# Optimization experiments

Measured on AMD Instinct MI355X. Metric: run time of the kernel, lower is better.

## Reference

```python
import jax, jax.numpy as jnp
import numpy as np

B, S, D, T = 32, 2048, 128, 8  # batch, seq, input_size, num_trans


def setup_inputs() -> dict:
    key = jax.random.key(0)
    k0, k1, k2, k3 = jax.random.split(key, 4)
    return {
        "input_data": jax.random.normal(k0, (B, S, D), dtype=jnp.float32),
        # nn.Linear(D, D) weights per transform, stacked: [T, D, D]
        "Wx": jax.random.normal(k1, (T, D, D), dtype=jnp.float32) / np.sqrt(D).astype(np.float32),
        "bx": jax.random.normal(k2, (T, D), dtype=jnp.float32) * 0.01,
        # torch.rand init in original
        "p_vectors": jax.random.uniform(k3, (T, 1, D), dtype=jnp.float32),
    }


def reference(input_data, Wx, bx, p_vectors):
    # Batched version of the Python loop of per-transform Linears.
    # torch Linear computes x @ W.T + b -> contract last dim of x with last dim of W.
    transformed = jnp.einsum('bsd,ted->tbse', input_data, Wx) + bx[:, None, None, :]  # [T,B,S,D]

    # Cosine-similarity gating against prototype vectors p_vectors [T,1,D].
    x_norm = jnp.linalg.norm(input_data, axis=2, keepdims=True)[None]        # [1,B,S,1]
    p_norm = jnp.linalg.norm(p_vectors, axis=2, keepdims=True)[:, None]      # [T,1,1,1]
    dot = jnp.sum(input_data[None] * p_vectors[:, None], axis=3, keepdims=True)  # [T,B,S,1]
    cos = dot / (x_norm * p_norm)
    sim = jax.nn.softmax(cos, axis=0)  # softmax over the T transforms

    # Weighted combine + residual (is_y=False path).
    return jnp.sum(sim * transformed, axis=0) + input_data  # [B,S,D]
```

## Files before the change

kernel.cpp:

```cpp
#include <hip/hip_runtime.h>

#define Tq 8
#define Mq 65536

typedef short bf16x8 __attribute__((ext_vector_type(8)));
typedef float f32x4 __attribute__((ext_vector_type(4)));

static __device__ __forceinline__ unsigned short f2bf(float f) {
    unsigned int u = __float_as_uint(f);
    unsigned int r = (u + 0x7FFFu + ((u >> 16) & 1u)) >> 16;
    return (unsigned short)r;
}

__global__ void prep_kernel(const float* __restrict__ W, const float* __restrict__ p,
                            unsigned short* __restrict__ ws) {
    int b = blockIdx.x;
    if (b < 512) {
        int i = b * 256 + threadIdx.x;
        int j    = i & 7;
        int lane = (i >> 3) & 63;
        int k    = (i >> 9) & 3;
        int n    = (i >> 11) & 7;
        int t    = i >> 14;
        int e = n * 16 + (lane & 15);
        int d = k * 32 + (lane >> 4) * 8 + j;
        float w = W[(t * 128 + e) * 128 + d];
        if (e == d) w += 1.0f;
        ws[i] = f2bf(w);
    } else {
        #pragma unroll
        for (int u = 0; u < 16; u++) {
            int i = u * 256 + threadIdx.x;
            int j    = i & 7;
            int lane = (i >> 3) & 63;
            int k    = i >> 9;
            int l16  = lane & 15;
            int quad = lane >> 4;
            int d = k * 32 + quad * 8 + j;
            float v = (l16 < Tq) ? p[l16 * 128 + d] : 0.0f;
            ws[131072 + i] = f2bf(v);
        }
    }
}

__global__ __launch_bounds__(256, 3) void main_kernel(const float* __restrict__ x,
                                                      const unsigned short* __restrict__ wsw,
                                                      const float* __restrict__ bx,
                                                      const float* __restrict__ p,
                                                      float* __restrict__ out) {
    __shared__ float bxl[Tq][64];
    __shared__ float pinv[Tq];

    int tid  = threadIdx.x;
    int bid  = blockIdx.x;
    int rb   = bid >> 1;
    int cb   = bid & 1;
    int wid  = tid >> 6;
    int lane = tid & 63;
    int l16  = lane & 15;
    int quad = lane >> 4;
    size_t wrow = (size_t)rb * 128 + wid * 32;

    {
        int c  = tid & 63;
        int t2 = tid >> 6;
        bxl[t2][c]     = bx[t2 * 128 + cb * 64 + c];
        bxl[t2 + 4][c] = bx[(t2 + 4) * 128 + cb * 64 + c];
    }
    if (tid < Tq) {
        const f32x4* pg = reinterpret_cast<const f32x4*>(p) + tid * 32;
        float s = 0.f;
        #pragma unroll
        for (int i = 0; i < 32; i++) {
            f32x4 v = pg[i];
            s += v.x * v.x + v.y * v.y + v.z * v.z + v.w * v.w;
        }
        pinv[tid] = rsqrtf(s);
    }

    bf16x8 a[2][4];
    float xinv[2];
    #pragma unroll
    for (int mt = 0; mt < 2; mt++) {
        const f32x4* xr = reinterpret_cast<const f32x4*>(x + (wrow + mt * 16 + l16) * 128);
        float ssq = 0.f;
        #pragma unroll
        for (int k = 0; k < 4; k++) {
            f32x4 v0 = __builtin_nontemporal_load(xr + k * 8 + quad * 2);
            f32x4 v1 = __builtin_nontemporal_load(xr + k * 8 + quad * 2 + 1);
            ssq += v0.x * v0.x + v0.y * v0.y + v0.z * v0.z + v0.w * v0.w
                 + v1.x * v1.x + v1.y * v1.y + v1.z * v1.z + v1.w * v1.w;
            bf16x8 f;
            f[0] = (short)f2bf(v0.x); f[1] = (short)f2bf(v0.y);
            f[2] = (short)f2bf(v0.z); f[3] = (short)f2bf(v0.w);
            f[4] = (short)f2bf(v1.x); f[5] = (short)f2bf(v1.y);
            f[6] = (short)f2bf(v1.z); f[7] = (short)f2bf(v1.w);
            a[mt][k] = f;
        }
        ssq += __shfl_xor(ssq, 16);
        ssq += __shfl_xor(ssq, 32);
        xinv[mt] = rsqrtf(ssq);
    }

    const bf16x8* pf = reinterpret_cast<const bf16x8*>(wsw) + 16384;
    bf16x8 pfrag[4];
    #pragma unroll
    for (int k = 0; k < 4; k++) pfrag[k] = pf[k * 64 + lane];
    f32x4 d[2] = {};
    #pragma unroll
    for (int k = 0; k < 4; k++) {
        d[0] = __builtin_amdgcn_mfma_f32_16x16x32_bf16(a[0][k], pfrag[k], d[0], 0, 0, 0);
        d[1] = __builtin_amdgcn_mfma_f32_16x16x32_bf16(a[1][k], pfrag[k], d[1], 0, 0, 0);
    }

    __syncthreads();

    float pv = pinv[l16 & 7];
    f32x4 sim[2];
    #pragma unroll
    for (int mt = 0; mt < 2; mt++) {
        f32x4 c;
        #pragma unroll
        for (int rr = 0; rr < 4; rr++) {
            float xir = __shfl(xinv[mt], (lane & 48) | (quad * 4 + rr));
            c[rr] = d[mt][rr] * xir * pv;
        }
        f32x4 mx = c;
        #pragma unroll
        for (int m = 1; m <= 4; m <<= 1)
            #pragma unroll
            for (int rr = 0; rr < 4; rr++) mx[rr] = fmaxf(mx[rr], __shfl_xor(mx[rr], m));
        f32x4 e;
        #pragma unroll
        for (int rr = 0; rr < 4; rr++) e[rr] = __expf(c[rr] - mx[rr]);
        f32x4 sm = e;
        #pragma unroll
        for (int m = 1; m <= 4; m <<= 1)
            #pragma unroll
            for (int rr = 0; rr < 4; rr++) sm[rr] += __shfl_xor(sm[rr], m);
        #pragma unroll
        for (int rr = 0; rr < 4; rr++) sim[mt][rr] = e[rr] / sm[rr];
    }

    const bf16x8* wb = reinterpret_cast<const bf16x8*>(wsw);
    int nt0 = cb * 4;
    bf16x8 buf[2][4];
    #pragma unroll
    for (int k = 0; k < 4; k++)
        buf[0][k] = wb[(size_t)((0 * 8 + nt0) * 4 + k) * 64 + lane];

    f32x4 o[2][4] = {};

    #pragma unroll 1
    for (int t = 0; t < Tq; t++) {
        f32x4 s0, s1;
        int src = (lane & 48) | t;
        #pragma unroll
        for (int rr = 0; rr < 4; rr++) {
            s0[rr] = __shfl(sim[0][rr], src);
            s1[rr] = __shfl(sim[1][rr], src);
        }
        #pragma unroll
        for (int n = 0; n < 4; n++) {
            int cur = n & 1;
            {
                int n2 = (n + 1) & 3;
                int t2 = (n == 3) ? ((t + 1) & 7) : t;
                #pragma unroll
                for (int k = 0; k < 4; k++)
                    buf[cur ^ 1][k] = wb[(size_t)((t2 * 8 + nt0 + n2) * 4 + k) * 64 + lane];
            }
            float bias = bxl[t][n * 16 + l16];
            f32x4 y0 = {bias, bias, bias, bias};
            f32x4 y1 = {bias, bias, bias, bias};
            #pragma unroll
            for (int k = 0; k < 4; k++) {
                y0 = __builtin_amdgcn_mfma_f32_16x16x32_bf16(a[0][k], buf[cur][k], y0, 0, 0, 0);
                y1 = __builtin_amdgcn_mfma_f32_16x16x32_bf16(a[1][k], buf[cur][k], y1, 0, 0, 0);
            }
            #pragma unroll
            for (int rr = 0; rr < 4; rr++) {
                o[0][n][rr] += s0[rr] * y0[rr];
                o[1][n][rr] += s1[rr] * y1[rr];
            }
        }
    }

    #pragma unroll
    for (int mt = 0; mt < 2; mt++)
        #pragma unroll
        for (int rr = 0; rr < 4; rr++) {
            size_t row = wrow + mt * 16 + quad * 4 + rr;
            #pragma unroll
            for (int n = 0; n < 4; n++)
                __builtin_nontemporal_store(o[mt][n][rr], out + row * 128 + cb * 64 + n * 16 + l16);
        }
}

extern "C" void kernel_launch(void* const* d_in, const int* in_sizes, int n_in,
                              void* d_out, int out_size, void* d_ws, size_t ws_size,
                              hipStream_t stream) {
    const float* x   = (const float*)d_in[0];
    const float* Wx  = (const float*)d_in[1];
    const float* bx  = (const float*)d_in[2];
    const float* p   = (const float*)d_in[3];
    float* out = (float*)d_out;

    unsigned short* ws = (unsigned short*)d_ws;

    prep_kernel<<<dim3(513), dim3(256), 0, stream>>>(Wx, p, ws);
    main_kernel<<<dim3(Mq / 128 * 2), dim3(256), 0, stream>>>(x, ws, bx, p, out);
}
```

Before: 124.7 us.

## Retile main kernel to 128-row blocks with LDS-staged x and double-buffered weights

Each block now covers 128 full rows instead of splitting output columns across two blocks, so x is read from global memory once instead of twice. x is converted to bf16 and staged in LDS, with row norms accumulated through shared atomics. Each wave computes a 64x64 tile with four M-subtiles. Per-transform weight tiles are brought in with global_load_lds into a double buffer in LDS instead of per-lane global loads. The cost is more registers, lower occupancy (launch bound 3 to 2), half as many blocks, and extra barriers per transform.

```diff
diff --git a/kernel.cpp b/kernel.cpp
--- a/kernel.cpp
+++ b/kernel.cpp
@@ -43,30 +43,28 @@
     }
 }
 
-__global__ __launch_bounds__(256, 3) void main_kernel(const float* __restrict__ x,
+__global__ __launch_bounds__(256, 2) void main_kernel(const float* __restrict__ x,
                                                       const unsigned short* __restrict__ wsw,
                                                       const float* __restrict__ bx,
                                                       const float* __restrict__ p,
                                                       float* __restrict__ out) {
-    __shared__ float bxl[Tq][64];
+    __shared__ unsigned short un[32768];
+    __shared__ float bxl[Tq][128];
+    __shared__ float ssql[128];
     __shared__ float pinv[Tq];
 
     int tid  = threadIdx.x;
-    int bid  = blockIdx.x;
-    int rb   = bid >> 1;
-    int cb   = bid & 1;
     int wid  = tid >> 6;
     int lane = tid & 63;
     int l16  = lane & 15;
     int quad = lane >> 4;
-    size_t wrow = (size_t)rb * 128 + wid * 32;
-
-    {
-        int c  = tid & 63;
-        int t2 = tid >> 6;
-        bxl[t2][c]     = bx[t2 * 128 + cb * 64 + c];
-        bxl[t2 + 4][c] = bx[(t2 + 4) * 128 + cb * 64 + c];
-    }
+    size_t m0 = (size_t)blockIdx.x * 128;
+    int mrow = (wid >> 1) * 64;
+    int nt0  = (wid & 1) * 4;
+    int ncol = (wid & 1) * 64;
+
+    if (tid < 128) ssql[tid] = 0.f;
+    reinterpret_cast<f32x4*>(&bxl[0][0])[tid] = reinterpret_cast<const f32x4*>(bx)[tid];
     if (tid < Tq) {
         const f32x4* pg = reinterpret_cast<const f32x4*>(p) + tid * 32;
         float s = 0.f;
@@ -77,123 +75,148 @@
         }
         pinv[tid] = rsqrtf(s);
     }
-
-    bf16x8 a[2][4];
-    float xinv[2];
-    #pragma unroll
-    for (int mt = 0; mt < 2; mt++) {
-        const f32x4* xr = reinterpret_cast<const f32x4*>(x + (wrow + mt * 16 + l16) * 128);
-        float ssq = 0.f;
-        #pragma unroll
-        for (int k = 0; k < 4; k++) {
-            f32x4 v0 = __builtin_nontemporal_load(xr + k * 8 + quad * 2);
-            f32x4 v1 = __builtin_nontemporal_load(xr + k * 8 + quad * 2 + 1);
-            ssq += v0.x * v0.x + v0.y * v0.y + v0.z * v0.z + v0.w * v0.w
-                 + v1.x * v1.x + v1.y * v1.y + v1.z * v1.z + v1.w * v1.w;
-            bf16x8 f;
-            f[0] = (short)f2bf(v0.x); f[1] = (short)f2bf(v0.y);
-            f[2] = (short)f2bf(v0.z); f[3] = (short)f2bf(v0.w);
-            f[4] = (short)f2bf(v1.x); f[5] = (short)f2bf(v1.y);
-            f[6] = (short)f2bf(v1.z); f[7] = (short)f2bf(v1.w);
-            a[mt][k] = f;
-        }
-        ssq += __shfl_xor(ssq, 16);
-        ssq += __shfl_xor(ssq, 32);
-        xinv[mt] = rsqrtf(ssq);
-    }
+    __syncthreads();
+
+    const f32x4* xg4 = reinterpret_cast<const f32x4*>(x + m0 * 128);
+    #pragma unroll
+    for (int it = 0; it < 16; it++) {
+        int flat = it * 256 + tid;
+        int row = flat >> 5;
+        int c4  = flat & 31;
+        f32x4 v = __builtin_nontemporal_load(xg4 + flat);
+        atomicAdd(&ssql[row], v.x * v.x + v.y * v.y + v.z * v.z + v.w * v.w);
+        ushort4 bv;
+        bv.x = f2bf(v.x); bv.y = f2bf(v.y); bv.z = f2bf(v.z); bv.w = f2bf(v.w);
+        *reinterpret_cast<ushort4*>(&un[row * 136 + c4 * 4]) = bv;
+    }
+    __syncthreads();
+
+    bf16x8 a[4][4];
+    #pragma unroll
+    for (int mt = 0; mt < 4; mt++)
+        #pragma unroll
+        for (int k = 0; k < 4; k++)
+            a[mt][k] = *reinterpret_cast<const bf16x8*>(&un[(mrow + mt * 16 + l16) * 136 + k * 32 + quad * 8]);
+
+    f32x4 xinvv[4];
+    #pragma unroll
+    for (int mt = 0; mt < 4; mt++)
+        #pragma unroll
+        for (int rr = 0; rr < 4; rr++)
+            xinvv[mt][rr] = rsqrtf(ssql[mrow + mt * 16 + quad * 4 + rr]);
 
     const bf16x8* pf = reinterpret_cast<const bf16x8*>(wsw) + 16384;
     bf16x8 pfrag[4];
     #pragma unroll
     for (int k = 0; k < 4; k++) pfrag[k] = pf[k * 64 + lane];
-    f32x4 d[2] = {};
-    #pragma unroll
-    for (int k = 0; k < 4; k++) {
-        d[0] = __builtin_amdgcn_mfma_f32_16x16x32_bf16(a[0][k], pfrag[k], d[0], 0, 0, 0);
-        d[1] = __builtin_amdgcn_mfma_f32_16x16x32_bf16(a[1][k], pfrag[k], d[1], 0, 0, 0);
-    }
+    f32x4 d[4] = {};
+    #pragma unroll
+    for (int k = 0; k < 4; k++)
+        #pragma unroll
+        for (int mt = 0; mt < 4; mt++)
+            d[mt] = __builtin_amdgcn_mfma_f32_16x16x32_bf16(a[mt][k], pfrag[k], d[mt], 0, 0, 0);
 
     __syncthreads();
 
+    const char* wsrc = reinterpret_cast<const char*>(wsw);
+    char* lbase = reinterpret_cast<char*>(un);
+    {
+        #pragma unroll
+        for (int it = 0; it < 8; it++) {
+            int off = it * 4096 + wid * 1024;
+            __builtin_amdgcn_global_load_lds(
+                (const __attribute__((address_space(1))) unsigned int*)(wsrc + off + lane * 16),
+                (__attribute__((address_space(3))) unsigned int*)(lbase + off),
+                16, 0, 0);
+        }
+    }
+
     float pv = pinv[l16 & 7];
-    f32x4 sim[2];
-    #pragma unroll
-    for (int mt = 0; mt < 2; mt++) {
+    f32x4 sim[4];
+    #pragma unroll
+    for (int mt = 0; mt < 4; mt++) {
         f32x4 c;
         #pragma unroll
-        for (int rr = 0; rr < 4; rr++) {
-            float xir = __shfl(xinv[mt], (lane & 48) | (quad * 4 + rr));
-            c[rr] = d[mt][rr] * xir * pv;
-        }
+        for (int rr = 0; rr < 4; rr++) c[rr] = d[mt][rr] * xinvv[mt][rr] * pv;
         f32x4 mx = c;
         #pragma unroll
         for (int m = 1; m <= 4; m <<= 1)
             #pragma unroll
             for (int rr = 0; rr < 4; rr++) mx[rr] = fmaxf(mx[rr], __shfl_xor(mx[rr], m));
-        f32x4 e;
-        #pragma unroll
-        for (int rr = 0; rr < 4; rr++) e[rr] = __expf(c[rr] - mx[rr]);
-        f32x4 sm = e;
+        #pragma unroll
+        for (int rr = 0; rr < 4; rr++) c[rr] = __expf(c[rr] - mx[rr]);
+        f32x4 sm = c;
         #pragma unroll
         for (int m = 1; m <= 4; m <<= 1)
             #pragma unroll
             for (int rr = 0; rr < 4; rr++) sm[rr] += __shfl_xor(sm[rr], m);
         #pragma unroll
-        for (int rr = 0; rr < 4; rr++) sim[mt][rr] = e[rr] / sm[rr];
-    }
-
-    const bf16x8* wb = reinterpret_cast<const bf16x8*>(wsw);
-    int nt0 = cb * 4;
-    bf16x8 buf[2][4];
-    #pragma unroll
-    for (int k = 0; k < 4; k++)
-        buf[0][k] = wb[(size_t)((0 * 8 + nt0) * 4 + k) * 64 + lane];
-
-    f32x4 o[2][4] = {};
-
+        for (int rr = 0; rr < 4; rr++) sim[mt][rr] = c[rr] / sm[rr];
+    }
+
+    f32x4 o[4][4] = {};
     #pragma unroll 1
     for (int t = 0; t < Tq; t++) {
-        f32x4 s0, s1;
+        __syncthreads();
+        if (t < 7) {
+            const char* ws2 = wsrc + (t + 1) * 32768;
+            char* ld2 = lbase + ((t + 1) & 1) * 32768;
+            #pragma unroll
+            for (int it = 0; it < 8; it++) {
+                int off = it * 4096 + wid * 1024;
+                __builtin_amdgcn_global_load_lds(
+                    (const __attribute__((address_space(1))) unsigned int*)(ws2 + off + lane * 16),
+                    (__attribute__((address_space(3))) unsigned int*)(ld2 + off),
+                    16, 0, 0);
+            }
+        }
+        f32x4 s[4];
         int src = (lane & 48) | t;
         #pragma unroll
-        for (int rr = 0; rr < 4; rr++) {
-            s0[rr] = __shfl(sim[0][rr], src);
-            s1[rr] = __shfl(sim[1][rr], src);
-        }
+        for (int mt = 0; mt < 4; mt++)
+            #pragma unroll
+            for (int rr = 0; rr < 4; rr++)
+                s[mt][rr] = __shfl(sim[mt][rr], src);
+
+        const unsigned short* wl = un + (t & 1) * 16384;
+        bf16x8 bfr[2][4];
+        #pragma unroll
+        for (int k = 0; k < 4; k++)
+            bfr[0][k] = *reinterpret_cast<const bf16x8*>(&wl[(((nt0) * 4 + k) * 64 + lane) * 8]);
+
         #pragma unroll
         for (int n = 0; n < 4; n++) {
             int cur = n & 1;
-            {
-                int n2 = (n + 1) & 3;
-                int t2 = (n == 3) ? ((t + 1) & 7) : t;
+            if (n < 3) {
                 #pragma unroll
                 for (int k = 0; k < 4; k++)
-                    buf[cur ^ 1][k] = wb[(size_t)((t2 * 8 + nt0 + n2) * 4 + k) * 64 + lane];
+                    bfr[cur ^ 1][k] = *reinterpret_cast<const bf16x8*>(&wl[(((nt0 + n + 1) * 4 + k) * 64 + lane) * 8]);
             }
-            float bias = bxl[t][n * 16 + l16];
-            f32x4 y0 = {bias, bias, bias, bias};
-            f32x4 y1 = {bias, bias, bias, bias};
-            #pragma unroll
-            for (int k = 0; k < 4; k++) {
-                y0 = __builtin_amdgcn_mfma_f32_16x16x32_bf16(a[0][k], buf[cur][k], y0, 0, 0, 0);
-                y1 = __builtin_amdgcn_mfma_f32_16x16x32_bf16(a[1][k], buf[cur][k], y1, 0, 0, 0);
-            }
-            #pragma unroll
-            for (int rr = 0; rr < 4; rr++) {
-                o[0][n][rr] += s0[rr] * y0[rr];
-                o[1][n][rr] += s1[rr] * y1[rr];
-            }
-        }
-    }
-
-    #pragma unroll
-    for (int mt = 0; mt < 2; mt++)
+            float bias = bxl[t][ncol + n * 16 + l16];
+            f32x4 y[4];
+            #pragma unroll
+            for (int mt = 0; mt < 4; mt++) y[mt] = (f32x4){bias, bias, bias, bias};
+            #pragma unroll
+            for (int k = 0; k < 4; k++)
+                #pragma unroll
+                for (int mt = 0; mt < 4; mt++)
+                    y[mt] = __builtin_amdgcn_mfma_f32_16x16x32_bf16(a[mt][k], bfr[cur][k], y[mt], 0, 0, 0);
+            #pragma unroll
+            for (int mt = 0; mt < 4; mt++)
+                #pragma unroll
+                for (int rr = 0; rr < 4; rr++)
+                    o[mt][n][rr] += s[mt][rr] * y[mt][rr];
+        }
+    }
+
+    #pragma unroll
+    for (int mt = 0; mt < 4; mt++)
         #pragma unroll
         for (int rr = 0; rr < 4; rr++) {
-            size_t row = wrow + mt * 16 + quad * 4 + rr;
+            size_t row = m0 + mrow + mt * 16 + quad * 4 + rr;
             #pragma unroll
             for (int n = 0; n < 4; n++)
-                __builtin_nontemporal_store(o[mt][n][rr], out + row * 128 + cb * 64 + n * 16 + l16);
+                __builtin_nontemporal_store(o[mt][n][rr], out + row * 128 + ncol + n * 16 + l16);
         }
 }
 
@@ -209,5 +232,5 @@
     unsigned short* ws = (unsigned short*)d_ws;
 
     prep_kernel<<<dim3(513), dim3(256), 0, stream>>>(Wx, p, ws);
-    main_kernel<<<dim3(Mq / 128 * 2), dim3(256), 0, stream>>>(x, ws, bx, p, out);
-}
+    main_kernel<<<dim3(Mq / 128), dim3(256), 0, stream>>>(x, ws, bx, p, out);
+}
```

Measured after the change: 122.8 us. Within noise of the previous version (-1.5%).
